# Kernel tuning notes

Hardware: AMD Instinct MI355X
Metric: run time of the kernel (lower is better)

## Reference

```python
import jax, jax.numpy as jnp
import numpy as np

D_MODEL = 2048
N_HEADS = 16
HEAD_DIM = D_MODEL // N_HEADS
D_FF = 4 * D_MODEL


def setup_inputs() -> dict:
    key = jax.random.key(0)
    ks = jax.random.split(key, 12)
    s = 1.0 / np.sqrt(D_MODEL)
    sf = 1.0 / np.sqrt(D_FF)
    return {
        "x": jax.random.normal(ks[0], (2, 2048, D_MODEL), dtype=jnp.float32),
        "wq": jax.random.uniform(ks[1], (D_MODEL, D_MODEL), jnp.float32, -s, s),
        "wk": jax.random.uniform(ks[2], (D_MODEL, D_MODEL), jnp.float32, -s, s),
        "wv": jax.random.uniform(ks[3], (D_MODEL, D_MODEL), jnp.float32, -s, s),
        "wo": jax.random.uniform(ks[4], (D_MODEL, D_MODEL), jnp.float32, -s, s),
        "w1": jax.random.uniform(ks[5], (D_MODEL, D_FF), jnp.float32, -s, s),
        "b1": jax.random.uniform(ks[6], (D_FF,), jnp.float32, -s, s),
        "w2": jax.random.uniform(ks[7], (D_FF, D_MODEL), jnp.float32, -sf, sf),
        "b2": jax.random.uniform(ks[8], (D_MODEL,), jnp.float32, -sf, sf),
        "g1": jnp.ones((D_MODEL,), jnp.float32),
        "be1": jnp.zeros((D_MODEL,), jnp.float32),
        "g2": jnp.ones((D_MODEL,), jnp.float32),
        "be2": jnp.zeros((D_MODEL,), jnp.float32),
    }


def _layernorm(x, g, b, eps=1e-5):
    mu = jnp.mean(x, axis=-1, keepdims=True)
    var = jnp.mean(jnp.square(x - mu), axis=-1, keepdims=True)
    return (x - mu) * jax.lax.rsqrt(var + eps) * g + b


def reference(x, wq, wk, wv, wo, w1, b1, w2, b2, g1, be1, g2, be2):
    B, S, D = x.shape
    residual = x
    h = _layernorm(x, g1, be1)
    # [B,S,D] -> [B,H,S,hd]
    q = (h @ wq).reshape(B, S, N_HEADS, HEAD_DIM).transpose(0, 2, 1, 3)
    k = (h @ wk).reshape(B, S, N_HEADS, HEAD_DIM).transpose(0, 2, 1, 3)
    v = (h @ wv).reshape(B, S, N_HEADS, HEAD_DIM).transpose(0, 2, 1, 3)
    scores = jnp.einsum("bhqd,bhkd->bhqk", q, k) / np.sqrt(HEAD_DIM).astype(np.float32)
    attn = jax.nn.softmax(scores, axis=-1)
    out = jnp.einsum("bhqk,bhkd->bhqd", attn, v)
    out = out.transpose(0, 2, 1, 3).reshape(B, S, D) @ wo
    x = residual + out
    residual = x
    h = _layernorm(x, g2, be2)
    h = jax.nn.gelu(h @ w1 + b1, approximate=False) @ w2 + b2
    return residual + h
```

## Files before the change

### kernel.cpp

```cpp
#include <hip/hip_runtime.h>
#include <cstdint>
#include <cstddef>

#define DM   2048
#define NH   16
#define HD   128
#define DFF  8192
#define SEQ  2048
#define NB   2
#define NTOK (NB * SEQ)

using bf16x8 = __attribute__((ext_vector_type(8))) __bf16;
using f32x4  = __attribute__((ext_vector_type(4))) float;

__device__ __forceinline__ unsigned short f2bf(float f) {
  unsigned int u = __float_as_uint(f);
  u += 0x7fffu + ((u >> 16) & 1u);
  return (unsigned short)(u >> 16);
}

__device__ __forceinline__ void gload16(const void* g, void* l) {
  __builtin_amdgcn_global_load_lds(
      (const __attribute__((address_space(1))) unsigned int*)g,
      (__attribute__((address_space(3))) unsigned int*)l, 16, 0, 0);
}

__device__ __forceinline__ f32x4 mfma16(bf16x8 a, bf16x8 b, f32x4 c) {
  return __builtin_amdgcn_mfma_f32_16x16x32_bf16(a, b, c, 0, 0, 0);
}

#define BARRIER() asm volatile("s_barrier" ::: "memory")
#define LGKM0()   asm volatile("s_waitcnt lgkmcnt(0)" ::: "memory")

__device__ __forceinline__ int xcd_swz(int hb, int nwg) {
  return (hb & 7) * (nwg >> 3) + (hb >> 3);
}

__global__ __launch_bounds__(256) void transpose_cast(
    const float* __restrict__ src, unsigned short* __restrict__ dst, int R, int C) {
  __shared__ float tile[32][33];
  const int r0 = blockIdx.y * 32, c0 = blockIdx.x * 32;
  const int tx = threadIdx.x, ty = threadIdx.y;
#pragma unroll
  for (int i = ty; i < 32; i += 8)
    tile[i][tx] = src[(size_t)(r0 + i) * C + c0 + tx];
  __syncthreads();
#pragma unroll
  for (int i = ty; i < 32; i += 8)
    dst[(size_t)(c0 + i) * R + r0 + tx] = f2bf(tile[tx][i]);
}

__global__ __launch_bounds__(256) void transpose_cast4(
    const float* __restrict__ wq, const float* __restrict__ wk,
    const float* __restrict__ wv, const float* __restrict__ wo,
    unsigned short* __restrict__ dqkv, unsigned short* __restrict__ dwo) {
  __shared__ float tile[32][33];
  const int z = blockIdx.z;
  const float* src = (z == 0) ? wq : (z == 1) ? wk : (z == 2) ? wv : wo;
  unsigned short* dst = (z < 3) ? (dqkv + (size_t)z * 2048 * 2048) : dwo;
  const int r0 = blockIdx.y * 32, c0 = blockIdx.x * 32;
  const int tx = threadIdx.x, ty = threadIdx.y;
#pragma unroll
  for (int i = ty; i < 32; i += 8)
    tile[i][tx] = src[(size_t)(r0 + i) * 2048 + c0 + tx];
  __syncthreads();
#pragma unroll
  for (int i = ty; i < 32; i += 8)
    dst[(size_t)(c0 + i) * 2048 + r0 + tx] = f2bf(tile[tx][i]);
}

__global__ __launch_bounds__(256) void ln_kernel(
    const float* __restrict__ x, const float* __restrict__ gam,
    const float* __restrict__ bet, unsigned short* __restrict__ out) {
  const int row = blockIdx.x, tid = threadIdx.x;
  const float* xr = x + (size_t)row * DM;
  float4 a = *(const float4*)(xr + tid * 8);
  float4 b = *(const float4*)(xr + tid * 8 + 4);
  float s  = a.x + a.y + a.z + a.w + b.x + b.y + b.z + b.w;
  float s2 = a.x*a.x + a.y*a.y + a.z*a.z + a.w*a.w +
             b.x*b.x + b.y*b.y + b.z*b.z + b.w*b.w;
#pragma unroll
  for (int off = 32; off > 0; off >>= 1) {
    s  += __shfl_xor(s, off);
    s2 += __shfl_xor(s2, off);
  }
  __shared__ float red[8];
  const int wid = tid >> 6;
  if ((tid & 63) == 0) { red[wid] = s; red[4 + wid] = s2; }
  __syncthreads();
  s  = red[0] + red[1] + red[2] + red[3];
  s2 = red[4] + red[5] + red[6] + red[7];
  const float mean = s * (1.0f / DM);
  const float var  = s2 * (1.0f / DM) - mean * mean;
  const float rstd = rsqrtf(var + 1e-5f);
  float4 g0 = *(const float4*)(gam + tid * 8);
  float4 g1 = *(const float4*)(gam + tid * 8 + 4);
  float4 e0 = *(const float4*)(bet + tid * 8);
  float4 e1 = *(const float4*)(bet + tid * 8 + 4);
  union { unsigned short u[8]; uint4 v; } pk;
  const float* av = (const float*)&a; const float* bv = (const float*)&b;
  const float* gv0 = (const float*)&g0; const float* gv1 = (const float*)&g1;
  const float* ev0 = (const float*)&e0; const float* ev1 = (const float*)&e1;
#pragma unroll
  for (int j = 0; j < 4; j++) pk.u[j]     = f2bf((av[j] - mean) * rstd * gv0[j] + ev0[j]);
#pragma unroll
  for (int j = 0; j < 4; j++) pk.u[4 + j] = f2bf((bv[j] - mean) * rstd * gv1[j] + ev1[j]);
  *(uint4*)(out + (size_t)row * DM + tid * 8) = pk.v;
}

template <int EPI>
__global__ __launch_bounds__(512, 2) void gemm256(
    const unsigned short* __restrict__ A, const unsigned short* __restrict__ Bt,
    int M, int N, int K,
    unsigned short* __restrict__ o0, unsigned short* __restrict__ o1,
    unsigned short* __restrict__ o2, float* __restrict__ fo,
    const float* __restrict__ e0, const float* __restrict__ e1) {
  __shared__ __attribute__((aligned(16))) unsigned short As[2][256 * 64];
  __shared__ __attribute__((aligned(16))) unsigned short Bs[2][256 * 64];
  const int tid = threadIdx.x;
  const int wid = tid >> 6, lane = tid & 63;
  const int wr = wid >> 2, wc = wid & 3;
  const int c16 = lane & 15, g = lane >> 4;
  const int m0 = blockIdx.y * 256, n0 = blockIdx.x * 256;

  const int c0 = tid, c1 = tid + 512;
  const int r0_ = c0 >> 3, s0_ = ((c0 & 7) ^ (r0_ & 7)) * 8;
  const int r1_ = c1 >> 3, s1_ = ((c1 & 7) ^ (r1_ & 7)) * 8;
  const unsigned short* a0p = A + (size_t)(m0 + r0_) * K + s0_;
  const unsigned short* a1p = A + (size_t)(m0 + r1_) * K + s1_;
  const unsigned short* b0p = Bt + (size_t)(n0 + r0_) * K + s0_;
  const unsigned short* b1p = Bt + (size_t)(n0 + r1_) * K + s1_;
  const size_t hstep = (size_t)128 * K;

  auto SA = [&](int buf, int h, int kt) {
    gload16(a0p + h * hstep + kt * 64, &As[buf][h * 8192 + c0 * 8]);
    gload16(a1p + h * hstep + kt * 64, &As[buf][h * 8192 + c1 * 8]);
  };
  auto SB = [&](int buf, int h, int kt) {
    gload16(b0p + h * hstep + kt * 64, &Bs[buf][h * 8192 + c0 * 8]);
    gload16(b1p + h * hstep + kt * 64, &Bs[buf][h * 8192 + c1 * 8]);
  };

  const int swz   = (c16 & 7) << 4;
  const int k0off = (g * 16) ^ swz;
  const int k1off = (64 + g * 16) ^ swz;

  f32x4 acc[8][4];
#pragma unroll
  for (int i = 0; i < 8; i++)
#pragma unroll
    for (int j = 0; j < 4; j++) acc[i][j] = f32x4{0.f, 0.f, 0.f, 0.f};

  bf16x8 af0[4][2], af1[4][2], bf0[2][2], bf1[2][2];

  const int NT = K >> 6;
  SA(0, 0, 0); SA(0, 1, 0); SB(0, 0, 0); SB(0, 1, 0);
  SB(1, 0, 1); SB(1, 1, 1); SA(1, 0, 1);
  asm volatile("s_waitcnt vmcnt(6)" ::: "memory");
  BARRIER();

  for (int t = 0; t < NT; ++t) {
    const int buf = t & 1;
    const char* Ac = (const char*)As[buf];
    const char* Bc = (const char*)Bs[buf];
    const bool st = (t + 2) < NT;
#pragma unroll
    for (int mi = 0; mi < 4; ++mi) {
      const int rb = (wr * 64 + mi * 16 + c16) * 128;
      af0[mi][0] = *(const bf16x8*)(Ac + rb + k0off);
      af0[mi][1] = *(const bf16x8*)(Ac + rb + k1off);
    }
#pragma unroll
    for (int ni = 0; ni < 2; ++ni) {
      const int rb = (wc * 32 + ni * 16 + c16) * 128;
      bf0[ni][0] = *(const bf16x8*)(Bc + rb + k0off);
      bf0[ni][1] = *(const bf16x8*)(Bc + rb + k1off);
    }
    if (t + 1 < NT) SA(buf ^ 1, 1, t + 1);
    BARRIER(); LGKM0();
    __builtin_amdgcn_s_setprio(1);
#pragma unroll
    for (int mi = 0; mi < 4; ++mi)
#pragma unroll
      for (int ni = 0; ni < 2; ++ni)
#pragma unroll
        for (int kk = 0; kk < 2; ++kk)
          acc[mi][ni] = mfma16(af0[mi][kk], bf0[ni][kk], acc[mi][ni]);
    __builtin_amdgcn_s_setprio(0);
    BARRIER();
#pragma unroll
    for (int ni = 0; ni < 2; ++ni) {
      const int rb = (128 + wc * 32 + ni * 16 + c16) * 128;
      bf1[ni][0] = *(const bf16x8*)(Bc + rb + k0off);
      bf1[ni][1] = *(const bf16x8*)(Bc + rb + k1off);
    }
    if (st) SB(buf, 0, t + 2);
    BARRIER(); LGKM0();
    __builtin_amdgcn_s_setprio(1);
#pragma unroll
    for (int mi = 0; mi < 4; ++mi)
#pragma unroll
      for (int ni = 0; ni < 2; ++ni)
#pragma unroll
        for (int kk = 0; kk < 2; ++kk)
          acc[mi][2 + ni] = mfma16(af0[mi][kk], bf1[ni][kk], acc[mi][2 + ni]);
    __builtin_amdgcn_s_setprio(0);
    BARRIER();
#pragma unroll
    for (int mi = 0; mi < 4; ++mi) {
      const int rb = (128 + wr * 64 + mi * 16 + c16) * 128;
      af1[mi][0] = *(const bf16x8*)(Ac + rb + k0off);
      af1[mi][1] = *(const bf16x8*)(Ac + rb + k1off);
    }
    if (st) SB(buf, 1, t + 2);
    BARRIER(); LGKM0();
    __builtin_amdgcn_s_setprio(1);
#pragma unroll
    for (int mi = 0; mi < 4; ++mi)
#pragma unroll
      for (int ni = 0; ni < 2; ++ni)
#pragma unroll
        for (int kk = 0; kk < 2; ++kk)
          acc[4 + mi][2 + ni] = mfma16(af1[mi][kk], bf1[ni][kk], acc[4 + mi][2 + ni]);
    __builtin_amdgcn_s_setprio(0);
    BARRIER();
    if (st) SA(buf, 0, t + 2);
    BARRIER();
    __builtin_amdgcn_s_setprio(1);
#pragma unroll
    for (int mi = 0; mi < 4; ++mi)
#pragma unroll
      for (int ni = 0; ni < 2; ++ni)
#pragma unroll
        for (int kk = 0; kk < 2; ++kk)
          acc[4 + mi][ni] = mfma16(af1[mi][kk], bf0[ni][kk], acc[4 + mi][ni]);
    __builtin_amdgcn_s_setprio(0);
    if (st) { asm volatile("s_waitcnt vmcnt(6)" ::: "memory"); }
    else    { asm volatile("s_waitcnt vmcnt(0)" ::: "memory"); }
    BARRIER();
  }

#pragma unroll
  for (int mi = 0; mi < 8; ++mi) {
    const int arow = (mi < 4) ? (wr * 64 + mi * 16) : (128 + wr * 64 + (mi - 4) * 16);
#pragma unroll
    for (int ni = 0; ni < 4; ++ni) {
      const int bcol = (ni < 2) ? (wc * 32 + ni * 16) : (128 + wc * 32 + (ni - 2) * 16);
#pragma unroll
      for (int r = 0; r < 4; ++r) {
        const int row = m0 + arow + g * 4 + r;
        const int col = n0 + bcol + c16;
        const float v = acc[mi][ni][r];
        if constexpr (EPI == 2) {
          const float t2 = v + e0[col];
          const float ge = 0.5f * t2 * (1.0f + erff(t2 * 0.7071067811865476f));
          o0[(size_t)row * N + col] = f2bf(ge);
        } else {
          const size_t idx = (size_t)row * N + col;
          fo[idx] = (EPI == 1) ? (e0[idx] + v) : (e1[idx] + v + e0[col]);
        }
      }
    }
  }
}

template <int EPI>
__global__ __launch_bounds__(256, 2) void gemm128(
    const unsigned short* __restrict__ A, const unsigned short* __restrict__ Bt,
    int M, int N, int K,
    unsigned short* __restrict__ o0, unsigned short* __restrict__ o1,
    unsigned short* __restrict__ o2, float* __restrict__ fo,
    const float* __restrict__ e0, const float* __restrict__ e1) {
  __shared__ __attribute__((aligned(16))) unsigned short SM[4][128 * 64];
  const int tid = threadIdx.x;
  const int wid = tid >> 6, lane = tid & 63;
  const int m0 = blockIdx.y * 128, n0 = blockIdx.x * 128;
  const int wr = wid >> 1, wc = wid & 1;
  const int c16 = lane & 15, g = lane >> 4;

  const unsigned short *ap[4], *bp[4];
  int dsto[4];
#pragma unroll
  for (int j = 0; j < 4; ++j) {
    const int c = tid + j * 256;
    const int r = c >> 3, s = ((c & 7) ^ (r & 7)) * 8;
    ap[j] = A + (size_t)(m0 + r) * K + s;
    bp[j] = Bt + (size_t)(n0 + r) * K + s;
    dsto[j] = c * 8;
  }
  auto SA = [&](int buf, int kt) {
#pragma unroll
    for (int j = 0; j < 4; ++j) gload16(ap[j] + kt * 64, &SM[buf][dsto[j]]);
  };
  auto SB = [&](int buf, int kt) {
#pragma unroll
    for (int j = 0; j < 4; ++j) gload16(bp[j] + kt * 64, &SM[2 + buf][dsto[j]]);
  };

  const int swz   = (c16 & 7) << 4;
  const int k0off = (g * 16) ^ swz;
  const int k1off = (64 + g * 16) ^ swz;

  f32x4 acc[4][4];
#pragma unroll
  for (int i = 0; i < 4; i++)
#pragma unroll
    for (int j = 0; j < 4; j++) acc[i][j] = f32x4{0.f, 0.f, 0.f, 0.f};

  bf16x8 af[4][2], bfm[4][2];

  const int NT = K >> 6;
  SA(0, 0); SB(0, 0);
  __syncthreads();

  for (int t = 0; t < NT; ++t) {
    const int buf = t & 1;
    const char* Ac = (const char*)SM[buf];
    const char* Bc = (const char*)SM[2 + buf];
    if (t + 1 < NT) { SA(buf ^ 1, t + 1); SB(buf ^ 1, t + 1); }
#pragma unroll
    for (int mi = 0; mi < 4; ++mi) {
      const int rb = (wr * 64 + mi * 16 + c16) * 128;
      af[mi][0] = *(const bf16x8*)(Ac + rb + k0off);
      af[mi][1] = *(const bf16x8*)(Ac + rb + k1off);
    }
#pragma unroll
    for (int ni = 0; ni < 4; ++ni) {
      const int rb = (wc * 64 + ni * 16 + c16) * 128;
      bfm[ni][0] = *(const bf16x8*)(Bc + rb + k0off);
      bfm[ni][1] = *(const bf16x8*)(Bc + rb + k1off);
    }
    __builtin_amdgcn_s_setprio(1);
#pragma unroll
    for (int mi = 0; mi < 4; ++mi)
#pragma unroll
      for (int ni = 0; ni < 4; ++ni)
#pragma unroll
        for (int kk = 0; kk < 2; ++kk)
          acc[mi][ni] = mfma16(af[mi][kk], bfm[ni][kk], acc[mi][ni]);
    __builtin_amdgcn_s_setprio(0);
    __syncthreads();
  }

  if constexpr (EPI == 0) {
    const int which = n0 >> 11;
    if (which == 2) {
      unsigned short* Ls = &SM[0][0];
#pragma unroll
      for (int mi = 0; mi < 4; ++mi)
#pragma unroll
        for (int ni = 0; ni < 4; ++ni)
#pragma unroll
          for (int r = 0; r < 4; ++r) {
            const int s_loc = wr * 64 + mi * 16 + g * 4 + r;
            const int d_loc = wc * 64 + ni * 16 + c16;
            Ls[d_loc * 136 + s_loc] = f2bf(acc[mi][ni][r]);
          }
      __syncthreads();
      const int b  = m0 >> 11, s0v = m0 & 2047;
      const int hh = (n0 & 2047) >> 7;
      const size_t base = (size_t)(b * NH + hh) * HD * (size_t)SEQ;
#pragma unroll
      for (int it2 = 0; it2 < 2; ++it2) {
        const int hd = it2 * 64 + (tid >> 2);
        const int sc = (tid & 3) * 32;
#pragma unroll
        for (int j = 0; j < 4; ++j) {
          uint4 vv = *(const uint4*)&Ls[hd * 136 + sc + j * 8];
          *(uint4*)&o2[base + (size_t)hd * SEQ + s0v + sc + j * 8] = vv;
        }
      }
    } else {
#pragma unroll
      for (int mi = 0; mi < 4; ++mi)
#pragma unroll
        for (int ni = 0; ni < 4; ++ni)
#pragma unroll
          for (int r = 0; r < 4; ++r) {
            const int row = m0 + wr * 64 + mi * 16 + g * 4 + r;
            const int col = n0 + wc * 64 + ni * 16 + c16;
            const float v = acc[mi][ni][r];
            const int b = row >> 11, s = row & 2047;
            const int d = col & 2047;
            const int hh = d >> 7, hd = d & 127;
            const size_t bh = (size_t)(b * NH + hh);
            if (which == 0) o0[(bh * SEQ + s) * HD + hd] = f2bf(v * 0.08838834764831845f);
            else            o1[(bh * SEQ + s) * HD + hd] = f2bf(v);
          }
    }
  } else {
#pragma unroll
    for (int mi = 0; mi < 4; ++mi) {
#pragma unroll
      for (int ni = 0; ni < 4; ++ni) {
#pragma unroll
        for (int r = 0; r < 4; ++r) {
          const int row = m0 + wr * 64 + mi * 16 + g * 4 + r;
          const int col = n0 + wc * 64 + ni * 16 + c16;
          const float v = acc[mi][ni][r];
          if constexpr (EPI == 2) {
            const float t2 = v + e0[col];
            const float ge = 0.5f * t2 * (1.0f + erff(t2 * 0.7071067811865476f));
            o0[(size_t)row * N + col] = f2bf(ge);
          } else {
            const size_t idx = (size_t)row * N + col;
            fo[idx] = (EPI == 1) ? (e0[idx] + v) : (e1[idx] + v + e0[col]);
          }
        }
      }
    }
  }
}

__global__ __launch_bounds__(256, 2) void attn_kernel(
    const unsigned short* __restrict__ q, const unsigned short* __restrict__ k,
    const unsigned short* __restrict__ vT, unsigned short* __restrict__ out) {
  __shared__ __attribute__((aligned(16))) unsigned short Ks[2][64 * 128];
  __shared__ __attribute__((aligned(16))) unsigned short Vs[2][128 * 64];
  __shared__ __attribute__((aligned(16))) unsigned short Ps[4 * 32 * 64];
  const int tid = threadIdx.x, wid = tid >> 6, lane = tid & 63;
  const int c16 = lane & 15, g = lane >> 4;
  const int vbk = xcd_swz(blockIdx.x, 512);
  const int qt = vbk & 15, h = (vbk >> 4) & 15, b = vbk >> 8;
  const int q0 = qt * 128;
  const unsigned short* qb = q + (size_t)(b * NH + h) * SEQ * HD;
  const unsigned short* kb = k + (size_t)(b * NH + h) * SEQ * HD;
  const unsigned short* vb = vT + (size_t)(b * NH + h) * HD * SEQ;

  bf16x8 aq[2][4];
#pragma unroll
  for (int mi = 0; mi < 2; mi++)
#pragma unroll
    for (int ks = 0; ks < 4; ks++)
      aq[mi][ks] = *(const bf16x8*)(qb + (size_t)(q0 + wid * 32 + mi * 16 + c16) * HD +
                                    ks * 32 + g * 8);

  f32x4 o[2][8] = {};
  float mrow[2][4], lrow[2][4];
#pragma unroll
  for (int mi = 0; mi < 2; mi++)
#pragma unroll
    for (int r = 0; r < 4; r++) { mrow[mi][r] = -1e30f; lrow[mi][r] = 0.f; }

  const int kRowB = tid >> 4;
  const int kChk  = (tid & 15) ^ (kRowB & 7);
  const int vRowB = tid >> 3;
  const int vChk  = (tid & 7) ^ (vRowB & 7);
  char* PsW = (char*)Ps + wid * 4096;

  auto STAGE = [&](int buf, int kv0) {
#pragma unroll
    for (int seg = 0; seg < 4; seg++) {
      gload16(kb + (size_t)(kv0 + seg * 16 + kRowB) * HD + kChk * 8,
              &Ks[buf][wid * 512 + seg * 2048]);
      gload16(vb + (size_t)(seg * 32 + vRowB) * SEQ + kv0 + vChk * 8,
              &Vs[buf][wid * 512 + seg * 2048]);
    }
  };

  STAGE(0, 0);
  __syncthreads();

  const int NIT = SEQ / 64;
  for (int it = 0; it < NIT; ++it) {
    const int cur = it & 1;
    if (it + 1 < NIT) STAGE(cur ^ 1, (it + 1) * 64);
    const char* Kc = (const char*)&Ks[cur][0];
    const char* Vc = (const char*)&Vs[cur][0];

    f32x4 sc[2][4] = {};
#pragma unroll
    for (int ks = 0; ks < 4; ks++) {
#pragma unroll
      for (int ni = 0; ni < 4; ni++) {
        const int kr = ni * 16 + c16;
        const int lin = kr * 256 + ks * 64 + g * 16;
        bf16x8 bk = *(const bf16x8*)(Kc + (lin ^ ((kr & 7) << 4)));
        sc[0][ni] = mfma16(aq[0][ks], bk, sc[0][ni]);
        sc[1][ni] = mfma16(aq[1][ks], bk, sc[1][ni]);
      }
    }

#pragma unroll
    for (int mi = 0; mi < 2; mi++) {
#pragma unroll
      for (int r = 0; r < 4; r++) {
        float pm = fmaxf(fmaxf(sc[mi][0][r], sc[mi][1][r]),
                         fmaxf(sc[mi][2][r], sc[mi][3][r]));
        pm = fmaxf(pm, __shfl_xor(pm, 1));
        pm = fmaxf(pm, __shfl_xor(pm, 2));
        pm = fmaxf(pm, __shfl_xor(pm, 4));
        pm = fmaxf(pm, __shfl_xor(pm, 8));
        if (!__all(pm <= mrow[mi][r])) {
          const float mnew = fmaxf(mrow[mi][r], pm);
          const float scal = __expf(mrow[mi][r] - mnew);
          mrow[mi][r] = mnew;
          lrow[mi][r] *= scal;
#pragma unroll
          for (int nj = 0; nj < 8; nj++) o[mi][nj][r] *= scal;
        }
        float rs = 0.f;
        const int prow = mi * 16 + g * 4 + r;
#pragma unroll
        for (int ni = 0; ni < 4; ni++) {
          const float p = __expf(sc[mi][ni][r] - mrow[mi][r]);
          rs += p;
          const int lin = prow * 128 + (ni * 16 + c16) * 2;
          *(unsigned short*)(PsW + (lin ^ ((prow & 7) << 4))) = f2bf(p);
        }
        rs += __shfl_xor(rs, 1);
        rs += __shfl_xor(rs, 2);
        rs += __shfl_xor(rs, 4);
        rs += __shfl_xor(rs, 8);
        lrow[mi][r] += rs;
      }
    }

#pragma unroll
    for (int ks2 = 0; ks2 < 2; ks2++) {
      bf16x8 pa[2];
#pragma unroll
      for (int mi = 0; mi < 2; mi++) {
        const int pr = mi * 16 + c16;
        const int lin = pr * 128 + ks2 * 64 + g * 16;
        pa[mi] = *(const bf16x8*)(PsW + (lin ^ ((pr & 7) << 4)));
      }
#pragma unroll
      for (int nj = 0; nj < 8; nj++) {
        const int vr = nj * 16 + c16;
        const int lin = vr * 128 + ks2 * 64 + g * 16;
        bf16x8 bv = *(const bf16x8*)(Vc + (lin ^ ((vr & 7) << 4)));
        o[0][nj] = mfma16(pa[0], bv, o[0][nj]);
        o[1][nj] = mfma16(pa[1], bv, o[1][nj]);
      }
    }
    __syncthreads();
  }

#pragma unroll
  for (int mi = 0; mi < 2; mi++)
#pragma unroll
    for (int r = 0; r < 4; r++) {
      const float inv = 1.0f / lrow[mi][r];
      const int s = q0 + wid * 32 + mi * 16 + g * 4 + r;
#pragma unroll
      for (int nj = 0; nj < 8; nj++)
        out[((size_t)(b * SEQ + s)) * DM + h * HD + nj * 16 + c16] =
            f2bf(o[mi][nj][r] * inv);
    }
}

extern "C" void kernel_launch(void* const* d_in, const int* in_sizes, int n_in,
                              void* d_out, int out_size, void* d_ws, size_t ws_size,
                              hipStream_t stream) {
  const float* x  = (const float*)d_in[0];
  const float* wq = (const float*)d_in[1];
  const float* wk = (const float*)d_in[2];
  const float* wv = (const float*)d_in[3];
  const float* wo = (const float*)d_in[4];
  const float* w1 = (const float*)d_in[5];
  const float* b1 = (const float*)d_in[6];
  const float* w2 = (const float*)d_in[7];
  const float* b2 = (const float*)d_in[8];
  const float* g1 = (const float*)d_in[9];
  const float* be1 = (const float*)d_in[10];
  const float* g2 = (const float*)d_in[11];
  const float* be2 = (const float*)d_in[12];

  char* ws = (char*)d_ws;
  unsigned short* wqkvT = (unsigned short*)(ws + 0);
  unsigned short* woT   = (unsigned short*)(ws + 25165824);
  unsigned short* w1T   = (unsigned short*)(ws + 33554432);
  unsigned short* w2T   = (unsigned short*)(ws + 67108864);
  float*          x2    = (float*)(ws + 100663296);
  unsigned short* hbuf  = (unsigned short*)(ws + 134217728);
  unsigned short* qbuf  = (unsigned short*)(ws + 150994944);
  unsigned short* kbuf  = (unsigned short*)(ws + 167772160);
  unsigned short* vtbuf = (unsigned short*)(ws + 184549376);
  unsigned short* ffh   = (unsigned short*)(ws + 150994944);

  const dim3 tb(32, 8);
  transpose_cast4<<<dim3(64, 64, 4), tb, 0, stream>>>(wq, wk, wv, wo, wqkvT, woT);
  transpose_cast<<<dim3(256, 64), tb, 0, stream>>>(w1, w1T, 2048, 8192);
  transpose_cast<<<dim3(64, 256), tb, 0, stream>>>(w2, w2T, 8192, 2048);

  ln_kernel<<<NTOK, 256, 0, stream>>>(x, g1, be1, hbuf);

  gemm128<0><<<dim3(48, 32), 256, 0, stream>>>(
      hbuf, wqkvT, NTOK, 6144, 2048, qbuf, kbuf, vtbuf, nullptr, nullptr, nullptr);

  attn_kernel<<<512, 256, 0, stream>>>(qbuf, kbuf, vtbuf, hbuf);

  gemm128<1><<<dim3(16, 32), 256, 0, stream>>>(
      hbuf, woT, NTOK, 2048, 2048, nullptr, nullptr, nullptr, x2, x, nullptr);

  ln_kernel<<<NTOK, 256, 0, stream>>>(x2, g2, be2, hbuf);

  gemm256<2><<<dim3(32, 16), 512, 0, stream>>>(
      hbuf, w1T, NTOK, DFF, 2048, ffh, nullptr, nullptr, nullptr, b1, nullptr);

  gemm128<3><<<dim3(16, 32), 256, 0, stream>>>(
      ffh, w2T, NTOK, 2048, DFF, nullptr, nullptr, nullptr, (float*)d_out, b2, x2);
}
```

Before: 670.1 us.

## Rewrite FFN1 GEMM with 16 waves and 32x32x16 MFMA tiles

Replaces the 512-thread 256x256 GEMM used for the W1+GELU projection with a 1024-thread version in which each of 16 waves owns a 64x64 sub-tile computed with 32x32x16 bf16 MFMAs instead of 16x16x32. Staging becomes a simple double buffer that loads the whole next K-tile at once, replacing the interleaved half-tile prefetch schedule. The intent is fewer LDS fragment reads per flop and more waves to hide latency. In exchange it loses the fine-grained load/compute interleave, waits for all loads each iteration, and the launch bound of 1024 threads with 4 waves per SIMD may limit registers per thread.

```diff
diff --git a/kernel.cpp b/kernel.cpp
--- a/kernel.cpp
+++ b/kernel.cpp
@@ -12,6 +12,7 @@
 
 using bf16x8 = __attribute__((ext_vector_type(8))) __bf16;
 using f32x4  = __attribute__((ext_vector_type(4))) float;
+using f32x16 = __attribute__((ext_vector_type(16))) float;
 
 __device__ __forceinline__ unsigned short f2bf(float f) {
   unsigned int u = __float_as_uint(f);
@@ -27,6 +28,9 @@
 
 __device__ __forceinline__ f32x4 mfma16(bf16x8 a, bf16x8 b, f32x4 c) {
   return __builtin_amdgcn_mfma_f32_16x16x32_bf16(a, b, c, 0, 0, 0);
+}
+__device__ __forceinline__ f32x16 mfma32(bf16x8 a, bf16x8 b, f32x16 c) {
+  return __builtin_amdgcn_mfma_f32_32x32x16_bf16(a, b, c, 0, 0, 0);
 }
 
 #define BARRIER() asm volatile("s_barrier" ::: "memory")
@@ -109,148 +113,92 @@
 }
 
 template <int EPI>
-__global__ __launch_bounds__(512, 2) void gemm256(
+__global__ __launch_bounds__(1024, 4) void gemm256w(
     const unsigned short* __restrict__ A, const unsigned short* __restrict__ Bt,
     int M, int N, int K,
-    unsigned short* __restrict__ o0, unsigned short* __restrict__ o1,
-    unsigned short* __restrict__ o2, float* __restrict__ fo,
+    unsigned short* __restrict__ o0, float* __restrict__ fo,
     const float* __restrict__ e0, const float* __restrict__ e1) {
   __shared__ __attribute__((aligned(16))) unsigned short As[2][256 * 64];
   __shared__ __attribute__((aligned(16))) unsigned short Bs[2][256 * 64];
   const int tid = threadIdx.x;
   const int wid = tid >> 6, lane = tid & 63;
   const int wr = wid >> 2, wc = wid & 3;
-  const int c16 = lane & 15, g = lane >> 4;
+  const int l31 = lane & 31, lh = lane >> 5;
   const int m0 = blockIdx.y * 256, n0 = blockIdx.x * 256;
 
-  const int c0 = tid, c1 = tid + 512;
+  const int c0 = tid, c1 = tid + 1024;
   const int r0_ = c0 >> 3, s0_ = ((c0 & 7) ^ (r0_ & 7)) * 8;
   const int r1_ = c1 >> 3, s1_ = ((c1 & 7) ^ (r1_ & 7)) * 8;
   const unsigned short* a0p = A + (size_t)(m0 + r0_) * K + s0_;
   const unsigned short* a1p = A + (size_t)(m0 + r1_) * K + s1_;
   const unsigned short* b0p = Bt + (size_t)(n0 + r0_) * K + s0_;
   const unsigned short* b1p = Bt + (size_t)(n0 + r1_) * K + s1_;
-  const size_t hstep = (size_t)128 * K;
-
-  auto SA = [&](int buf, int h, int kt) {
-    gload16(a0p + h * hstep + kt * 64, &As[buf][h * 8192 + c0 * 8]);
-    gload16(a1p + h * hstep + kt * 64, &As[buf][h * 8192 + c1 * 8]);
+
+  auto STAGE = [&](int buf, int kt) {
+    gload16(a0p + kt * 64, &As[buf][c0 * 8]);
+    gload16(a1p + kt * 64, &As[buf][c1 * 8]);
+    gload16(b0p + kt * 64, &Bs[buf][c0 * 8]);
+    gload16(b1p + kt * 64, &Bs[buf][c1 * 8]);
   };
-  auto SB = [&](int buf, int h, int kt) {
-    gload16(b0p + h * hstep + kt * 64, &Bs[buf][h * 8192 + c0 * 8]);
-    gload16(b1p + h * hstep + kt * 64, &Bs[buf][h * 8192 + c1 * 8]);
-  };
-
-  const int swz   = (c16 & 7) << 4;
-  const int k0off = (g * 16) ^ swz;
-  const int k1off = (64 + g * 16) ^ swz;
-
-  f32x4 acc[8][4];
-#pragma unroll
-  for (int i = 0; i < 8; i++)
-#pragma unroll
-    for (int j = 0; j < 4; j++) acc[i][j] = f32x4{0.f, 0.f, 0.f, 0.f};
-
-  bf16x8 af0[4][2], af1[4][2], bf0[2][2], bf1[2][2];
+
+  const int swz = (l31 & 7) << 4;
+  const int arb0 = (wr * 64 + l31) * 128, arb1 = (wr * 64 + 32 + l31) * 128;
+  const int brb0 = (wc * 64 + l31) * 128, brb1 = (wc * 64 + 32 + l31) * 128;
+
+  f32x16 acc[2][2];
+#pragma unroll
+  for (int i = 0; i < 2; ++i)
+#pragma unroll
+    for (int j = 0; j < 2; ++j)
+#pragma unroll
+      for (int r = 0; r < 16; ++r) acc[i][j][r] = 0.f;
+
+  bf16x8 af[2][2], bf[2][2];
 
   const int NT = K >> 6;
-  SA(0, 0, 0); SA(0, 1, 0); SB(0, 0, 0); SB(0, 1, 0);
-  SB(1, 0, 1); SB(1, 1, 1); SA(1, 0, 1);
-  asm volatile("s_waitcnt vmcnt(6)" ::: "memory");
+  STAGE(0, 0);
+  asm volatile("s_waitcnt vmcnt(0)" ::: "memory");
   BARRIER();
 
   for (int t = 0; t < NT; ++t) {
     const int buf = t & 1;
     const char* Ac = (const char*)As[buf];
     const char* Bc = (const char*)Bs[buf];
-    const bool st = (t + 2) < NT;
-#pragma unroll
-    for (int mi = 0; mi < 4; ++mi) {
-      const int rb = (wr * 64 + mi * 16 + c16) * 128;
-      af0[mi][0] = *(const bf16x8*)(Ac + rb + k0off);
-      af0[mi][1] = *(const bf16x8*)(Ac + rb + k1off);
-    }
-#pragma unroll
-    for (int ni = 0; ni < 2; ++ni) {
-      const int rb = (wc * 32 + ni * 16 + c16) * 128;
-      bf0[ni][0] = *(const bf16x8*)(Bc + rb + k0off);
-      bf0[ni][1] = *(const bf16x8*)(Bc + rb + k1off);
-    }
-    if (t + 1 < NT) SA(buf ^ 1, 1, t + 1);
-    BARRIER(); LGKM0();
-    __builtin_amdgcn_s_setprio(1);
-#pragma unroll
-    for (int mi = 0; mi < 4; ++mi)
-#pragma unroll
-      for (int ni = 0; ni < 2; ++ni)
-#pragma unroll
-        for (int kk = 0; kk < 2; ++kk)
-          acc[mi][ni] = mfma16(af0[mi][kk], bf0[ni][kk], acc[mi][ni]);
-    __builtin_amdgcn_s_setprio(0);
-    BARRIER();
-#pragma unroll
-    for (int ni = 0; ni < 2; ++ni) {
-      const int rb = (128 + wc * 32 + ni * 16 + c16) * 128;
-      bf1[ni][0] = *(const bf16x8*)(Bc + rb + k0off);
-      bf1[ni][1] = *(const bf16x8*)(Bc + rb + k1off);
-    }
-    if (st) SB(buf, 0, t + 2);
-    BARRIER(); LGKM0();
-    __builtin_amdgcn_s_setprio(1);
-#pragma unroll
-    for (int mi = 0; mi < 4; ++mi)
-#pragma unroll
-      for (int ni = 0; ni < 2; ++ni)
-#pragma unroll
-        for (int kk = 0; kk < 2; ++kk)
-          acc[mi][2 + ni] = mfma16(af0[mi][kk], bf1[ni][kk], acc[mi][2 + ni]);
-    __builtin_amdgcn_s_setprio(0);
-    BARRIER();
-#pragma unroll
-    for (int mi = 0; mi < 4; ++mi) {
-      const int rb = (128 + wr * 64 + mi * 16 + c16) * 128;
-      af1[mi][0] = *(const bf16x8*)(Ac + rb + k0off);
-      af1[mi][1] = *(const bf16x8*)(Ac + rb + k1off);
-    }
-    if (st) SB(buf, 1, t + 2);
-    BARRIER(); LGKM0();
-    __builtin_amdgcn_s_setprio(1);
-#pragma unroll
-    for (int mi = 0; mi < 4; ++mi)
-#pragma unroll
-      for (int ni = 0; ni < 2; ++ni)
-#pragma unroll
-        for (int kk = 0; kk < 2; ++kk)
-          acc[4 + mi][2 + ni] = mfma16(af1[mi][kk], bf1[ni][kk], acc[4 + mi][2 + ni]);
-    __builtin_amdgcn_s_setprio(0);
-    BARRIER();
-    if (st) SA(buf, 0, t + 2);
-    BARRIER();
-    __builtin_amdgcn_s_setprio(1);
-#pragma unroll
-    for (int mi = 0; mi < 4; ++mi)
-#pragma unroll
-      for (int ni = 0; ni < 2; ++ni)
-#pragma unroll
-        for (int kk = 0; kk < 2; ++kk)
-          acc[4 + mi][ni] = mfma16(af1[mi][kk], bf0[ni][kk], acc[4 + mi][ni]);
-    __builtin_amdgcn_s_setprio(0);
-    if (st) { asm volatile("s_waitcnt vmcnt(6)" ::: "memory"); }
-    else    { asm volatile("s_waitcnt vmcnt(0)" ::: "memory"); }
-    BARRIER();
-  }
-
-#pragma unroll
-  for (int mi = 0; mi < 8; ++mi) {
-    const int arow = (mi < 4) ? (wr * 64 + mi * 16) : (128 + wr * 64 + (mi - 4) * 16);
-#pragma unroll
-    for (int ni = 0; ni < 4; ++ni) {
-      const int bcol = (ni < 2) ? (wc * 32 + ni * 16) : (128 + wc * 32 + (ni - 2) * 16);
-#pragma unroll
-      for (int r = 0; r < 4; ++r) {
-        const int row = m0 + arow + g * 4 + r;
-        const int col = n0 + bcol + c16;
-        const float v = acc[mi][ni][r];
+    if (t + 1 < NT) STAGE(buf ^ 1, t + 1);
+#pragma unroll
+    for (int p = 0; p < 2; ++p) {
+#pragma unroll
+      for (int s = 0; s < 2; ++s) {
+        const int ko = (((p * 2 + s) * 32 + lh * 16) ^ swz);
+        af[0][s] = *(const bf16x8*)(Ac + arb0 + ko);
+        af[1][s] = *(const bf16x8*)(Ac + arb1 + ko);
+        bf[0][s] = *(const bf16x8*)(Bc + brb0 + ko);
+        bf[1][s] = *(const bf16x8*)(Bc + brb1 + ko);
+      }
+      BARRIER(); LGKM0();
+      __builtin_amdgcn_s_setprio(1);
+#pragma unroll
+      for (int s = 0; s < 2; ++s)
+#pragma unroll
+        for (int ar = 0; ar < 2; ++ar)
+#pragma unroll
+          for (int br = 0; br < 2; ++br)
+            acc[ar][br] = mfma32(af[ar][s], bf[br][s], acc[ar][br]);
+      __builtin_amdgcn_s_setprio(0);
+      if (p == 1) { asm volatile("s_waitcnt vmcnt(0)" ::: "memory"); }
+      BARRIER();
+    }
+  }
+
+#pragma unroll
+  for (int ar = 0; ar < 2; ++ar) {
+#pragma unroll
+    for (int br = 0; br < 2; ++br) {
+#pragma unroll
+      for (int reg = 0; reg < 16; ++reg) {
+        const int row = m0 + wr * 64 + ar * 32 + (reg & 3) + 8 * (reg >> 2) + 4 * lh;
+        const int col = n0 + wc * 64 + br * 32 + l31;
+        const float v = acc[ar][br][reg];
         if constexpr (EPI == 2) {
           const float t2 = v + e0[col];
           const float ge = 0.5f * t2 * (1.0f + erff(t2 * 0.7071067811865476f));
@@ -596,8 +544,8 @@
 
   ln_kernel<<<NTOK, 256, 0, stream>>>(x2, g2, be2, hbuf);
 
-  gemm256<2><<<dim3(32, 16), 512, 0, stream>>>(
-      hbuf, w1T, NTOK, DFF, 2048, ffh, nullptr, nullptr, nullptr, b1, nullptr);
+  gemm256w<2><<<dim3(32, 16), 1024, 0, stream>>>(
+      hbuf, w1T, NTOK, DFF, 2048, ffh, nullptr, b1, nullptr);
 
   gemm128<3><<<dim3(16, 32), 256, 0, stream>>>(
       ffh, w2T, NTOK, 2048, DFF, nullptr, nullptr, nullptr, (float*)d_out, b2, x2);
```

New measurement: 702.0 us. 4.8% more time.
